# Optimization experiments

Hardware: AMD Instinct MI355X
Metric: run time of the kernel (lower is better)

Reference implementation:

```python
import jax, jax.numpy as jnp
import numpy as np

N_NODES = 50000
N_EDGES = 800000
IN_CH = 256
HID_CH = 128


def setup_inputs() -> dict:
    key = jax.random.key(0)
    k1, k2, k3, k4, k5 = jax.random.split(key, 5)
    x = jax.random.normal(k1, (N_NODES, IN_CH), dtype=jnp.float32)
    edge_index = jax.random.randint(k2, (2, N_EDGES), 0, N_NODES, dtype=jnp.int64)
    edge_weight = jax.random.uniform(k3, (N_EDGES,), dtype=jnp.float32)
    W = jax.random.normal(k4, (IN_CH, HID_CH), dtype=jnp.float32) * (1.0 / np.sqrt(IN_CH))
    b = jnp.zeros((HID_CH,), dtype=jnp.float32)
    alpha = jnp.full((HID_CH,), 0.25, dtype=jnp.float32)  # PReLU default init
    return {"x": x, "edge_index": edge_index, "edge_weight": edge_weight,
            "W": W, "b": b, "alpha": alpha}


def reference(x, edge_index, edge_weight, W, b, alpha):
    """GCNConv (with self-loops + symmetric normalization) followed by PReLU."""
    N = x.shape[0]
    row, col = edge_index[0], edge_index[1]
    # add self-loops with weight 1 (PyG gcn_norm default, add_self_loops=True)
    loop = jnp.arange(N, dtype=row.dtype)
    row = jnp.concatenate([row, loop])
    col = jnp.concatenate([col, loop])
    ew = jnp.concatenate([edge_weight, jnp.ones((N,), dtype=edge_weight.dtype)])
    # degree from edge weights, scattered at destination (col)
    deg = jax.ops.segment_sum(ew, col, num_segments=N)
    deg_inv_sqrt = jnp.where(deg > 0, jax.lax.rsqrt(deg), 0.0)
    norm = deg_inv_sqrt[row] * ew * deg_inv_sqrt[col]  # [E+N]
    # linear transform then gather-scale-scatter aggregation
    h = x @ W                               # [N, HID]
    msg = h[row] * norm[:, None]            # [E+N, HID]
    out = jax.ops.segment_sum(msg, col, num_segments=N) + b
    # PReLU with per-channel slope
    return jnp.where(out >= 0, out, alpha * out)
```

## Files before the change

kernel.cpp:

```cpp
#include <hip/hip_runtime.h>

#define NN 50000
#define NE 800000
#define KD 256
#define CD 128
#define NB 196

typedef __attribute__((ext_vector_type(8))) short short8;
typedef __attribute__((ext_vector_type(4))) float floatx4;

__device__ inline unsigned short f2bf(float f) {
    unsigned u = __float_as_uint(f);
    unsigned r = (u + 0x7FFFu + ((u >> 16) & 1u)) >> 16;
    return (unsigned short)r;
}
__device__ inline float bf2f_lo(unsigned u) { return __uint_as_float(u << 16); }
__device__ inline float bf2f_hi(unsigned u) { return __uint_as_float(u & 0xFFFF0000u); }

__global__ __launch_bounds__(256) void deg_hist(const int* __restrict__ col,
                                                const float* __restrict__ ew,
                                                unsigned long long* __restrict__ packed,
                                                unsigned short* __restrict__ rank) {
    int e = blockIdx.x * 256 + threadIdx.x;
    if (e < NE) {
        unsigned long long p = (1ull << 40)
                             + (unsigned long long)(ew[e] * 4294967296.0f);
        unsigned long long old = atomicAdd(&packed[col[e]], p);
        rank[e] = (unsigned short)(old >> 40);
    }
}

__global__ __launch_bounds__(256) void scan_blocks(const unsigned long long* __restrict__ packed,
                                                   int* __restrict__ local,
                                                   int* __restrict__ partials) {
    __shared__ int sm[256];
    const int t = threadIdx.x;
    const int g = blockIdx.x * 256 + t;
    int v = (g < NN) ? (int)(packed[g] >> 40) : 0;
    sm[t] = v;
    __syncthreads();
#pragma unroll
    for (int off = 1; off < 256; off <<= 1) {
        int u = (t >= off) ? sm[t - off] : 0;
        __syncthreads();
        sm[t] += u;
        __syncthreads();
    }
    local[g] = sm[t] - v;
    if (t == 255) partials[blockIdx.x] = sm[t];
}

__global__ __launch_bounds__(256) void scan_partials(int* __restrict__ partials) {
    __shared__ int sm[256];
    const int t = threadIdx.x;
    int v = (t < NB) ? partials[t] : 0;
    sm[t] = v;
    __syncthreads();
#pragma unroll
    for (int off = 1; off < 256; off <<= 1) {
        int u = (t >= off) ? sm[t - off] : 0;
        __syncthreads();
        sm[t] += u;
        __syncthreads();
    }
    if (t < NB) partials[t] = sm[t] - v;
}

__global__ __launch_bounds__(256) void scan_apply(const int* __restrict__ local,
                                                  const int* __restrict__ partials,
                                                  const unsigned long long* __restrict__ packed,
                                                  int* __restrict__ start,
                                                  float* __restrict__ dinv) {
    const int g = blockIdx.x * 256 + threadIdx.x;
    if (g < NN) {
        start[g] = local[g] + partials[blockIdx.x];
        float degs = (float)(packed[g] & ((1ull << 40) - 1)) * (1.0f / 4294967296.0f);
        dinv[g] = rsqrtf(1.0f + degs);
    }
    if (g == 0) start[NN] = NE;
}

__global__ __launch_bounds__(256) void meta_write(const int* __restrict__ row,
                                                  const int* __restrict__ col,
                                                  const float* __restrict__ ew,
                                                  const unsigned short* __restrict__ rank,
                                                  const int* __restrict__ start,
                                                  const float* __restrict__ dinv,
                                                  int2* __restrict__ meta) {
    int e = blockIdx.x * 256 + threadIdx.x;
    if (e >= NE) return;
    int c = col[e];
    int r = row[e];
    int pos = start[c] + rank[e];
    float f = dinv[r] * ew[e];
    meta[pos] = make_int2(r, __float_as_int(f));
}

__global__ __launch_bounds__(256) void w_transpose(const float* __restrict__ W,
                                                   unsigned short* __restrict__ Wt) {
    __shared__ unsigned short t[32][33];
    const int bk = blockIdx.x * 32;
    const int bn = blockIdx.y * 32;
    const int tx = threadIdx.x & 31;
    const int ty = threadIdx.x >> 5;
#pragma unroll
    for (int i = 0; i < 32; i += 8)
        t[ty + i][tx] = f2bf(W[(size_t)(bk + ty + i) * CD + bn + tx]);
    __syncthreads();
#pragma unroll
    for (int i = 0; i < 32; i += 8)
        Wt[(size_t)(bn + ty + i) * KD + bk + tx] = t[tx][ty + i];
}

__global__ __launch_bounds__(256) void gemm_mfma(const float* __restrict__ x,
                                                 const unsigned short* __restrict__ Wt,
                                                 unsigned short* __restrict__ hb) {
    __shared__ unsigned short As[64][40];
    __shared__ unsigned short Bs[128][40];

    const int tid  = threadIdx.x;
    const int wave = tid >> 6;
    const int lane = tid & 63;
    const int row0 = blockIdx.x * 64;
    const int m0   = wave * 16;
    const int lr   = lane & 15;
    const int quad = lane >> 4;

    const int ar = tid >> 2;
    const int aq = tid & 3;
    const int bn = tid >> 1;
    const int bh = (tid & 1) * 16;

    floatx4 acc[8];
#pragma unroll
    for (int nt = 0; nt < 8; nt++) acc[nt] = (floatx4){0.f, 0.f, 0.f, 0.f};

    for (int kt = 0; kt < 8; kt++) {
        const int k0 = kt * 32;
        union { short8 v; unsigned short u[8]; } av;
        const int gr = row0 + ar;
        if (gr < NN) {
            const float* xp = x + (size_t)gr * KD + k0 + aq * 8;
            float4 f0 = *(const float4*)xp;
            float4 f1 = *(const float4*)(xp + 4);
            av.u[0] = f2bf(f0.x); av.u[1] = f2bf(f0.y);
            av.u[2] = f2bf(f0.z); av.u[3] = f2bf(f0.w);
            av.u[4] = f2bf(f1.x); av.u[5] = f2bf(f1.y);
            av.u[6] = f2bf(f1.z); av.u[7] = f2bf(f1.w);
        } else {
            av.v = (short8){0,0,0,0,0,0,0,0};
        }
        *(short8*)&As[ar][aq * 8] = av.v;
        const unsigned short* wp = Wt + (size_t)bn * KD + k0 + bh;
        *(short8*)&Bs[bn][bh]     = *(const short8*)wp;
        *(short8*)&Bs[bn][bh + 8] = *(const short8*)(wp + 8);
        __syncthreads();
        short8 af = *(const short8*)&As[m0 + lr][quad * 8];
#pragma unroll
        for (int nt = 0; nt < 8; nt++) {
            short8 bfr = *(const short8*)&Bs[nt * 16 + lr][quad * 8];
            acc[nt] = __builtin_amdgcn_mfma_f32_16x16x32_bf16(af, bfr, acc[nt], 0, 0, 0);
        }
        __syncthreads();
    }

#pragma unroll
    for (int i = 0; i < 4; i++) {
        const int grow = row0 + m0 + quad * 4 + i;
        if (grow < NN) {
            unsigned short* hp = hb + (size_t)grow * CD + lr;
#pragma unroll
            for (int nt = 0; nt < 8; nt++)
                hp[nt * 16] = f2bf(acc[nt][i]);
        }
    }
}

__global__ __launch_bounds__(256) void aggregate(const int* __restrict__ start,
                                                 const int2* __restrict__ meta,
                                                 const unsigned short* __restrict__ hb,
                                                 const float* __restrict__ dinv,
                                                 const float* __restrict__ bias,
                                                 const float* __restrict__ alpha,
                                                 float* __restrict__ out) {
    int n = blockIdx.x * 4 + (threadIdx.x >> 6);
    if (n >= NN) return;
    n = __builtin_amdgcn_readfirstlane(n);
    const int lane = threadIdx.x & 63;
    const int s = __builtin_amdgcn_readfirstlane(start[n]);
    const int e = __builtin_amdgcn_readfirstlane(start[n + 1]);

    float a0 = 0.f, a1 = 0.f, b0 = 0.f, b1 = 0.f;
    float c0 = 0.f, c1 = 0.f, d0 = 0.f, d1 = 0.f;
    int i = s;
    for (; i + 4 <= e; i += 4) {
        int2 m0 = meta[i], m1 = meta[i + 1], m2 = meta[i + 2], m3 = meta[i + 3];
        unsigned u0 = *(const unsigned*)(hb + (size_t)m0.x * CD + lane * 2);
        unsigned u1 = *(const unsigned*)(hb + (size_t)m1.x * CD + lane * 2);
        unsigned u2 = *(const unsigned*)(hb + (size_t)m2.x * CD + lane * 2);
        unsigned u3 = *(const unsigned*)(hb + (size_t)m3.x * CD + lane * 2);
        float w0 = __int_as_float(m0.y), w1 = __int_as_float(m1.y);
        float w2 = __int_as_float(m2.y), w3 = __int_as_float(m3.y);
        a0 = fmaf(w0, bf2f_lo(u0), a0); a1 = fmaf(w0, bf2f_hi(u0), a1);
        b0 = fmaf(w1, bf2f_lo(u1), b0); b1 = fmaf(w1, bf2f_hi(u1), b1);
        c0 = fmaf(w2, bf2f_lo(u2), c0); c1 = fmaf(w2, bf2f_hi(u2), c1);
        d0 = fmaf(w3, bf2f_lo(u3), d0); d1 = fmaf(w3, bf2f_hi(u3), d1);
    }
    for (; i < e; i++) {
        int2 m = meta[i];
        unsigned u = *(const unsigned*)(hb + (size_t)m.x * CD + lane * 2);
        float w = __int_as_float(m.y);
        a0 = fmaf(w, bf2f_lo(u), a0);
        a1 = fmaf(w, bf2f_hi(u), a1);
    }
    a0 += b0 + c0 + d0;
    a1 += b1 + c1 + d1;

    const float dc = dinv[n];
    unsigned us = *(const unsigned*)(hb + (size_t)n * CD + lane * 2);
    const int ch = lane * 2;
    float o0 = dc * a0 + dc * dc * bf2f_lo(us) + bias[ch];
    float o1 = dc * a1 + dc * dc * bf2f_hi(us) + bias[ch + 1];
    o0 = o0 >= 0.f ? o0 : alpha[ch] * o0;
    o1 = o1 >= 0.f ? o1 : alpha[ch + 1] * o1;
    *(float2*)(out + (size_t)n * CD + ch) = make_float2(o0, o1);
}

extern "C" void kernel_launch(void* const* d_in, const int* in_sizes, int n_in,
                              void* d_out, int out_size, void* d_ws, size_t ws_size,
                              hipStream_t stream) {
    const float* x     = (const float*)d_in[0];
    const int*   eidx  = (const int*)d_in[1];
    const float* ew    = (const float*)d_in[2];
    const float* Wm    = (const float*)d_in[3];
    const float* bias  = (const float*)d_in[4];
    const float* alpha = (const float*)d_in[5];
    const int* row = eidx;
    const int* col = eidx + NE;

    float* out = (float*)d_out;

    char* ws = (char*)d_ws;
    unsigned long long* packed = (unsigned long long*)(ws);
    int*   start    = (int*)(ws + 400000);
    int*   local    = (int*)(ws + 600016);
    int*   partials = (int*)(ws + 800720);
    float* dinv     = (float*)(ws + 801504);
    unsigned short* rank = (unsigned short*)(ws + 1001504);
    int2*  meta     = (int2*)(ws + 2601504);
    unsigned short* Wt = (unsigned short*)(ws + 9001504);
    unsigned short* hb = (unsigned short*)(ws + 9067040);

    hipMemsetAsync(ws, 0, 400000, stream);
    deg_hist     <<<(NE + 255) / 256, 256, 0, stream>>>(col, ew, packed, rank);
    scan_blocks  <<<NB, 256, 0, stream>>>(packed, local, partials);
    scan_partials<<<1, 256, 0, stream>>>(partials);
    scan_apply   <<<NB, 256, 0, stream>>>(local, partials, packed, start, dinv);
    w_transpose  <<<dim3(8, 4), 256, 0, stream>>>(Wm, Wt);
    gemm_mfma    <<<(NN + 63) / 64, 256, 0, stream>>>(x, Wt, hb);
    meta_write   <<<(NE + 255) / 256, 256, 0, stream>>>(row, col, ew, rank, start, dinv, meta);
    aggregate    <<<(NN + 3) / 4, 256, 0, stream>>>(start, meta, hb, dinv, bias, alpha, out);
}
```

Baseline: 216.8 us.

## Fuse GEMM with degree histogram, fold partial scan into apply, unroll aggregation 8x

Merges the independent degree-histogram atomics and the bf16 MFMA GEMM into one launch that splits work by block index, so the atomic-bound histogram can overlap with the compute-bound GEMM. Drops the single-block scan_partials kernel by having each scan_apply block reduce the partials preceding it. Widens the aggregate gather unroll from 4 to 8 independent accumulators to keep more loads in flight. The fused kernel reserves GEMM shared memory even for histogram blocks, and the extra accumulators raise register pressure.

Result: faster. 205.5 us (-5.2%).

```diff
diff --git a/kernel.cpp b/kernel.cpp
--- a/kernel.cpp
+++ b/kernel.cpp
@@ -5,6 +5,8 @@
 #define KD 256
 #define CD 128
 #define NB 196
+#define GEMM_BLOCKS 782
+#define HIST_BLOCKS 3125
 
 typedef __attribute__((ext_vector_type(8))) short short8;
 typedef __attribute__((ext_vector_type(4))) float floatx4;
@@ -17,16 +19,80 @@
 __device__ inline float bf2f_lo(unsigned u) { return __uint_as_float(u << 16); }
 __device__ inline float bf2f_hi(unsigned u) { return __uint_as_float(u & 0xFFFF0000u); }
 
-__global__ __launch_bounds__(256) void deg_hist(const int* __restrict__ col,
-                                                const float* __restrict__ ew,
-                                                unsigned long long* __restrict__ packed,
-                                                unsigned short* __restrict__ rank) {
-    int e = blockIdx.x * 256 + threadIdx.x;
-    if (e < NE) {
-        unsigned long long p = (1ull << 40)
-                             + (unsigned long long)(ew[e] * 4294967296.0f);
-        unsigned long long old = atomicAdd(&packed[col[e]], p);
-        rank[e] = (unsigned short)(old >> 40);
+__global__ __launch_bounds__(256) void fused_gemm_hist(
+        const float* __restrict__ x, const unsigned short* __restrict__ Wt,
+        unsigned short* __restrict__ hb,
+        const int* __restrict__ col, const float* __restrict__ ew,
+        unsigned long long* __restrict__ packed, unsigned short* __restrict__ rank) {
+    __shared__ unsigned short As[64][40];
+    __shared__ unsigned short Bs[128][40];
+
+    if (blockIdx.x >= GEMM_BLOCKS) {
+        int e = (blockIdx.x - GEMM_BLOCKS) * 256 + threadIdx.x;
+        if (e < NE) {
+            unsigned long long p = (1ull << 40)
+                                 + (unsigned long long)(ew[e] * 4294967296.0f);
+            unsigned long long old = atomicAdd(&packed[col[e]], p);
+            rank[e] = (unsigned short)(old >> 40);
+        }
+        return;
+    }
+
+    const int tid  = threadIdx.x;
+    const int wave = tid >> 6;
+    const int lane = tid & 63;
+    const int row0 = blockIdx.x * 64;
+    const int m0   = wave * 16;
+    const int lr   = lane & 15;
+    const int quad = lane >> 4;
+
+    const int ar = tid >> 2;
+    const int aq = tid & 3;
+    const int bn = tid >> 1;
+    const int bh = (tid & 1) * 16;
+
+    floatx4 acc[8];
+#pragma unroll
+    for (int nt = 0; nt < 8; nt++) acc[nt] = (floatx4){0.f, 0.f, 0.f, 0.f};
+
+    for (int kt = 0; kt < 8; kt++) {
+        const int k0 = kt * 32;
+        union { short8 v; unsigned short u[8]; } av;
+        const int gr = row0 + ar;
+        if (gr < NN) {
+            const float* xp = x + (size_t)gr * KD + k0 + aq * 8;
+            float4 f0 = *(const float4*)xp;
+            float4 f1 = *(const float4*)(xp + 4);
+            av.u[0] = f2bf(f0.x); av.u[1] = f2bf(f0.y);
+            av.u[2] = f2bf(f0.z); av.u[3] = f2bf(f0.w);
+            av.u[4] = f2bf(f1.x); av.u[5] = f2bf(f1.y);
+            av.u[6] = f2bf(f1.z); av.u[7] = f2bf(f1.w);
+        } else {
+            av.v = (short8){0,0,0,0,0,0,0,0};
+        }
+        *(short8*)&As[ar][aq * 8] = av.v;
+        const unsigned short* wp = Wt + (size_t)bn * KD + k0 + bh;
+        *(short8*)&Bs[bn][bh]     = *(const short8*)wp;
+        *(short8*)&Bs[bn][bh + 8] = *(const short8*)(wp + 8);
+        __syncthreads();
+        short8 af = *(const short8*)&As[m0 + lr][quad * 8];
+#pragma unroll
+        for (int nt = 0; nt < 8; nt++) {
+            short8 bfr = *(const short8*)&Bs[nt * 16 + lr][quad * 8];
+            acc[nt] = __builtin_amdgcn_mfma_f32_16x16x32_bf16(af, bfr, acc[nt], 0, 0, 0);
+        }
+        __syncthreads();
+    }
+
+#pragma unroll
+    for (int i = 0; i < 4; i++) {
+        const int grow = row0 + m0 + quad * 4 + i;
+        if (grow < NN) {
+            unsigned short* hp = hb + (size_t)grow * CD + lr;
+#pragma unroll
+            for (int nt = 0; nt < 8; nt++)
+                hp[nt * 16] = f2bf(acc[nt][i]);
+        }
     }
 }
 
@@ -50,30 +116,25 @@
     if (t == 255) partials[blockIdx.x] = sm[t];
 }
 
-__global__ __launch_bounds__(256) void scan_partials(int* __restrict__ partials) {
-    __shared__ int sm[256];
-    const int t = threadIdx.x;
-    int v = (t < NB) ? partials[t] : 0;
-    sm[t] = v;
-    __syncthreads();
-#pragma unroll
-    for (int off = 1; off < 256; off <<= 1) {
-        int u = (t >= off) ? sm[t - off] : 0;
-        __syncthreads();
-        sm[t] += u;
-        __syncthreads();
-    }
-    if (t < NB) partials[t] = sm[t] - v;
-}
-
 __global__ __launch_bounds__(256) void scan_apply(const int* __restrict__ local,
                                                   const int* __restrict__ partials,
                                                   const unsigned long long* __restrict__ packed,
                                                   int* __restrict__ start,
                                                   float* __restrict__ dinv) {
-    const int g = blockIdx.x * 256 + threadIdx.x;
+    __shared__ int sm[256];
+    const int t = threadIdx.x;
+    const int b = blockIdx.x;
+    sm[t] = (t < b) ? partials[t] : 0;
+    __syncthreads();
+#pragma unroll
+    for (int off = 128; off > 0; off >>= 1) {
+        if (t < off) sm[t] += sm[t + off];
+        __syncthreads();
+    }
+    const int base = sm[0];
+    const int g = b * 256 + t;
     if (g < NN) {
-        start[g] = local[g] + partials[blockIdx.x];
+        start[g] = local[g] + base;
         float degs = (float)(packed[g] & ((1ull << 40) - 1)) * (1.0f / 4294967296.0f);
         dinv[g] = rsqrtf(1.0f + degs);
     }
@@ -112,70 +173,6 @@
         Wt[(size_t)(bn + ty + i) * KD + bk + tx] = t[tx][ty + i];
 }
 
-__global__ __launch_bounds__(256) void gemm_mfma(const float* __restrict__ x,
-                                                 const unsigned short* __restrict__ Wt,
-                                                 unsigned short* __restrict__ hb) {
-    __shared__ unsigned short As[64][40];
-    __shared__ unsigned short Bs[128][40];
-
-    const int tid  = threadIdx.x;
-    const int wave = tid >> 6;
-    const int lane = tid & 63;
-    const int row0 = blockIdx.x * 64;
-    const int m0   = wave * 16;
-    const int lr   = lane & 15;
-    const int quad = lane >> 4;
-
-    const int ar = tid >> 2;
-    const int aq = tid & 3;
-    const int bn = tid >> 1;
-    const int bh = (tid & 1) * 16;
-
-    floatx4 acc[8];
-#pragma unroll
-    for (int nt = 0; nt < 8; nt++) acc[nt] = (floatx4){0.f, 0.f, 0.f, 0.f};
-
-    for (int kt = 0; kt < 8; kt++) {
-        const int k0 = kt * 32;
-        union { short8 v; unsigned short u[8]; } av;
-        const int gr = row0 + ar;
-        if (gr < NN) {
-            const float* xp = x + (size_t)gr * KD + k0 + aq * 8;
-            float4 f0 = *(const float4*)xp;
-            float4 f1 = *(const float4*)(xp + 4);
-            av.u[0] = f2bf(f0.x); av.u[1] = f2bf(f0.y);
-            av.u[2] = f2bf(f0.z); av.u[3] = f2bf(f0.w);
-            av.u[4] = f2bf(f1.x); av.u[5] = f2bf(f1.y);
-            av.u[6] = f2bf(f1.z); av.u[7] = f2bf(f1.w);
-        } else {
-            av.v = (short8){0,0,0,0,0,0,0,0};
-        }
-        *(short8*)&As[ar][aq * 8] = av.v;
-        const unsigned short* wp = Wt + (size_t)bn * KD + k0 + bh;
-        *(short8*)&Bs[bn][bh]     = *(const short8*)wp;
-        *(short8*)&Bs[bn][bh + 8] = *(const short8*)(wp + 8);
-        __syncthreads();
-        short8 af = *(const short8*)&As[m0 + lr][quad * 8];
-#pragma unroll
-        for (int nt = 0; nt < 8; nt++) {
-            short8 bfr = *(const short8*)&Bs[nt * 16 + lr][quad * 8];
-            acc[nt] = __builtin_amdgcn_mfma_f32_16x16x32_bf16(af, bfr, acc[nt], 0, 0, 0);
-        }
-        __syncthreads();
-    }
-
-#pragma unroll
-    for (int i = 0; i < 4; i++) {
-        const int grow = row0 + m0 + quad * 4 + i;
-        if (grow < NN) {
-            unsigned short* hp = hb + (size_t)grow * CD + lr;
-#pragma unroll
-            for (int nt = 0; nt < 8; nt++)
-                hp[nt * 16] = f2bf(acc[nt][i]);
-        }
-    }
-}
-
 __global__ __launch_bounds__(256) void aggregate(const int* __restrict__ start,
                                                  const int2* __restrict__ meta,
                                                  const unsigned short* __restrict__ hb,
@@ -190,37 +187,41 @@
     const int s = __builtin_amdgcn_readfirstlane(start[n]);
     const int e = __builtin_amdgcn_readfirstlane(start[n + 1]);
 
-    float a0 = 0.f, a1 = 0.f, b0 = 0.f, b1 = 0.f;
-    float c0 = 0.f, c1 = 0.f, d0 = 0.f, d1 = 0.f;
+    float A0[8], A1[8];
+#pragma unroll
+    for (int j = 0; j < 8; j++) { A0[j] = 0.f; A1[j] = 0.f; }
+
     int i = s;
-    for (; i + 4 <= e; i += 4) {
-        int2 m0 = meta[i], m1 = meta[i + 1], m2 = meta[i + 2], m3 = meta[i + 3];
-        unsigned u0 = *(const unsigned*)(hb + (size_t)m0.x * CD + lane * 2);
-        unsigned u1 = *(const unsigned*)(hb + (size_t)m1.x * CD + lane * 2);
-        unsigned u2 = *(const unsigned*)(hb + (size_t)m2.x * CD + lane * 2);
-        unsigned u3 = *(const unsigned*)(hb + (size_t)m3.x * CD + lane * 2);
-        float w0 = __int_as_float(m0.y), w1 = __int_as_float(m1.y);
-        float w2 = __int_as_float(m2.y), w3 = __int_as_float(m3.y);
-        a0 = fmaf(w0, bf2f_lo(u0), a0); a1 = fmaf(w0, bf2f_hi(u0), a1);
-        b0 = fmaf(w1, bf2f_lo(u1), b0); b1 = fmaf(w1, bf2f_hi(u1), b1);
-        c0 = fmaf(w2, bf2f_lo(u2), c0); c1 = fmaf(w2, bf2f_hi(u2), c1);
-        d0 = fmaf(w3, bf2f_lo(u3), d0); d1 = fmaf(w3, bf2f_hi(u3), d1);
+    for (; i + 8 <= e; i += 8) {
+        int2 m[8];
+        unsigned u[8];
+#pragma unroll
+        for (int j = 0; j < 8; j++) m[j] = meta[i + j];
+#pragma unroll
+        for (int j = 0; j < 8; j++)
+            u[j] = *(const unsigned*)(hb + (size_t)m[j].x * CD + lane * 2);
+#pragma unroll
+        for (int j = 0; j < 8; j++) {
+            float w = __int_as_float(m[j].y);
+            A0[j] = fmaf(w, bf2f_lo(u[j]), A0[j]);
+            A1[j] = fmaf(w, bf2f_hi(u[j]), A1[j]);
+        }
     }
     for (; i < e; i++) {
         int2 m = meta[i];
         unsigned u = *(const unsigned*)(hb + (size_t)m.x * CD + lane * 2);
         float w = __int_as_float(m.y);
-        a0 = fmaf(w, bf2f_lo(u), a0);
-        a1 = fmaf(w, bf2f_hi(u), a1);
-    }
-    a0 += b0 + c0 + d0;
-    a1 += b1 + c1 + d1;
+        A0[0] = fmaf(w, bf2f_lo(u), A0[0]);
+        A1[0] = fmaf(w, bf2f_hi(u), A1[0]);
+    }
+#pragma unroll
+    for (int j = 1; j < 8; j++) { A0[0] += A0[j]; A1[0] += A1[j]; }
 
     const float dc = dinv[n];
     unsigned us = *(const unsigned*)(hb + (size_t)n * CD + lane * 2);
     const int ch = lane * 2;
-    float o0 = dc * a0 + dc * dc * bf2f_lo(us) + bias[ch];
-    float o1 = dc * a1 + dc * dc * bf2f_hi(us) + bias[ch + 1];
+    float o0 = dc * A0[0] + dc * dc * bf2f_lo(us) + bias[ch];
+    float o1 = dc * A1[0] + dc * dc * bf2f_hi(us) + bias[ch + 1];
     o0 = o0 >= 0.f ? o0 : alpha[ch] * o0;
     o1 = o1 >= 0.f ? o1 : alpha[ch + 1] * o1;
     *(float2*)(out + (size_t)n * CD + ch) = make_float2(o0, o1);
@@ -252,12 +253,11 @@
     unsigned short* hb = (unsigned short*)(ws + 9067040);
 
     hipMemsetAsync(ws, 0, 400000, stream);
-    deg_hist     <<<(NE + 255) / 256, 256, 0, stream>>>(col, ew, packed, rank);
-    scan_blocks  <<<NB, 256, 0, stream>>>(packed, local, partials);
-    scan_partials<<<1, 256, 0, stream>>>(partials);
-    scan_apply   <<<NB, 256, 0, stream>>>(local, partials, packed, start, dinv);
-    w_transpose  <<<dim3(8, 4), 256, 0, stream>>>(Wm, Wt);
-    gemm_mfma    <<<(NN + 63) / 64, 256, 0, stream>>>(x, Wt, hb);
-    meta_write   <<<(NE + 255) / 256, 256, 0, stream>>>(row, col, ew, rank, start, dinv, meta);
-    aggregate    <<<(NN + 3) / 4, 256, 0, stream>>>(start, meta, hb, dinv, bias, alpha, out);
-}
+    w_transpose   <<<dim3(8, 4), 256, 0, stream>>>(Wm, Wt);
+    fused_gemm_hist<<<GEMM_BLOCKS + HIST_BLOCKS, 256, 0, stream>>>(
+                        x, Wt, hb, col, ew, packed, rank);
+    scan_blocks   <<<NB, 256, 0, stream>>>(packed, local, partials);
+    scan_apply    <<<NB, 256, 0, stream>>>(local, partials, packed, start, dinv);
+    meta_write    <<<(NE + 255) / 256, 256, 0, stream>>>(row, col, ew, rank, start, dinv, meta);
+    aggregate     <<<(NN + 3) / 4, 256, 0, stream>>>(start, meta, hb, dinv, bias, alpha, out);
+}
```
